# Kernel optimization log

Measured on AMD Instinct MI355X. Metric: run time of the kernel, lower is better.

## Reference

```python
import jax, jax.numpy as jnp
import numpy as np
from jax import lax

DIM = 256
RATE = 4
MAX_SK_IT = 10
N = RATE
NC = N * DIM            # 1024
NG = N * N + 2 * N      # 24


def setup_inputs() -> dict:
    key = jax.random.key(0)
    ks = jax.random.split(key, 5)
    h = jax.random.normal(ks[0], (8, 4096, N, DIM), jnp.float32)
    norm_weight = jax.random.normal(ks[1], (NC,), jnp.float32)
    w = jax.random.normal(ks[2], (NC, NG), jnp.float32) * 0.02
    alpha = jax.random.normal(ks[3], (3,), jnp.float32) * 0.01
    beta = jax.random.normal(ks[4], (NG,), jnp.float32) * 0.1
    return {"h": h, "norm_weight": norm_weight, "w": w, "alpha": alpha, "beta": beta}


def _sinkhorn(K, iters):
    # Sinkhorn-Knopp diagonal scalings u, v such that diag(u) @ K @ diag(v)
    # is (approximately) doubly stochastic. K: (BL, N, N) positive.
    BL, n, _ = K.shape
    u = jnp.ones((BL, n), K.dtype)
    v = jnp.ones((BL, n), K.dtype)

    def body(carry, _):
        u, v = carry
        u = 1.0 / (jnp.einsum('bij,bj->bi', K, v) + 1e-8)
        v = 1.0 / (jnp.einsum('bij,bi->bj', K, u) + 1e-8)
        return (u, v), None

    (u, v), _ = lax.scan(body, (u, v), None, length=iters)
    return u, v


def reference(h, norm_weight, w, alpha, beta):
    B, L, n, D = h.shape
    hf = h.reshape(B, L, n * D)              # (B,L,NC)
    hv = norm_weight * hf                    # mapping uses raw norm weight
    H = hv @ w                               # (B,L,NG)
    r = jnp.linalg.norm(hf, axis=-1, keepdims=True) / np.float32(np.sqrt(n * D))
    r_ = 1.0 / (r + 1e-6)

    H_pre = jax.nn.sigmoid(r_ * H[..., :n] * alpha[0] + beta[:n])            # (B,L,N)
    H_post = 2.0 * jax.nn.sigmoid(r_ * H[..., n:2 * n] * alpha[1] + beta[n:2 * n])
    H_res = (r_ * H[..., 2 * n:] * alpha[2] + beta[2 * n:]).reshape(B, L, n, n)

    K = jnp.exp(H_res).reshape(B * L, n, n)
    u, v = _sinkhorn(K, MAX_SK_IT)
    u = lax.stop_gradient(u)
    v = lax.stop_gradient(v)
    P = (u[:, :, None] * K * v[:, None, :]).reshape(B, L, n, n)

    # process
    h_pre = jnp.einsum('bln,blnd->bld', H_pre, h)[:, :, None, :]  # (B,L,1,D)
    h_res = jnp.einsum('blnm,blmd->blnd', P, h)                   # (B,L,N,D)

    # depth_connection with h_out = h_pre (identity inner layer)
    out = H_post[..., None] * h_pre + h_res                       # (B,L,N,D)
    return out
```

## Files before the change

kernel.cpp:

```cpp
#include <hip/hip_runtime.h>
#include <math.h>


#define NTOK 8

typedef __attribute__((ext_vector_type(2))) _Float16 h2v;

__device__ __forceinline__ float fdot2f(unsigned int a, unsigned int b, float c) {
#if __has_builtin(__builtin_amdgcn_fdot2)
    return __builtin_amdgcn_fdot2(__builtin_bit_cast(h2v, a),
                                  __builtin_bit_cast(h2v, b), c, false);
#else
    h2v av = __builtin_bit_cast(h2v, a);
    h2v bv = __builtin_bit_cast(h2v, b);
    return fmaf((float)av[1], (float)bv[1],
           fmaf((float)av[0], (float)bv[0], c));
#endif
}

__device__ __forceinline__ unsigned int pk_f16(float a, float b) {
    const auto p = __builtin_amdgcn_cvt_pkrtz(a, b);
    return __builtin_bit_cast(unsigned int, p);
}

__device__ __forceinline__ float sigmoid_f(float z) {
    return 1.0f / (1.0f + __expf(-z));
}

__device__ __forceinline__ float row16_sum(float x) {
    x += __int_as_float(__builtin_amdgcn_update_dpp(
        0, __float_as_int(x), 0x121, 0xf, 0xf, false));
    x += __int_as_float(__builtin_amdgcn_update_dpp(
        0, __float_as_int(x), 0x122, 0xf, 0xf, false));
    x += __int_as_float(__builtin_amdgcn_update_dpp(
        0, __float_as_int(x), 0x124, 0xf, 0xf, false));
    x += __int_as_float(__builtin_amdgcn_update_dpp(
        0, __float_as_int(x), 0x128, 0xf, 0xf, false));
    return x;
}

__global__ __launch_bounds__(256)
void prep_kernel(const float* __restrict__ nw,
                 const float* __restrict__ w,
                 const float* __restrict__ alpha,
                 unsigned short* __restrict__ wt)
{
    const int tid = blockIdx.x * 256 + threadIdx.x;
    const int flat = 4 * tid;
    const float4 w4 = *(const float4*)(w + flat);
    const float a0 = alpha[0], a1 = alpha[1], a2 = alpha[2];
    const float vals[4] = {w4.x, w4.y, w4.z, w4.w};
    #pragma unroll
    for (int c = 0; c < 4; ++c) {
        const int f = flat + c;
        const int k = f / 24;
        const int n = f - 24 * k;
        const float as = (n < 4) ? a0 : ((n < 8) ? a1 : a2);
        const unsigned int p = pk_f16(as * nw[k] * vals[c], 0.f);
        wt[n * 1024 + k] = (unsigned short)(p & 0xffffu);
    }
}

__global__ __launch_bounds__(256)
void mhc_kernel(const float* __restrict__ h,
                const unsigned short* __restrict__ wt,
                const float* __restrict__ beta,
                float* __restrict__ out)
{
    const int tid  = threadIdx.x;
    const int lane = tid & 63;
    const int wv   = tid >> 6;
    const int ksl  = lane & 15;
    const int ng   = lane >> 4;

    __shared__ unsigned int tile[NTOK * 512];
    __shared__ float Hpart[NTOK][28];
    __shared__ float smalls[NTOK][26];

    const long tok0 = (long)blockIdx.x * NTOK;

    {
        const float* src = h + tok0 * 1024 + 4 * tid;
        #pragma unroll
        for (int i = 0; i < NTOK; ++i) {
            const float4 v = *(const float4*)(src + 1024 * i);
            uint2 u;
            u.x = pk_f16(v.x, v.y);
            u.y = pk_f16(v.z, v.w);
            *(uint2*)(tile + i * 512 + 2 * tid) = u;
        }
    }
    __syncthreads();

    const int t0 = 2 * wv;
    const uint4* txp = (const uint4*)tile + t0 * 128 + ksl;
    const uint4* twp = (const uint4*)wt + (6 * ng) * 128 + ksl;

    float acc[2][6], r2[2];
    #pragma unroll
    for (int t = 0; t < 2; ++t) {
        r2[t] = 0.f;
        #pragma unroll
        for (int j = 0; j < 6; ++j) acc[t][j] = 0.f;
    }

    #pragma unroll 1
    for (int e = 0; e < 8; ++e) {
        uint4 xw[2];
        #pragma unroll
        for (int t = 0; t < 2; ++t) xw[t] = txp[t * 128 + e * 16];
        uint4 wr[6];
        #pragma unroll
        for (int j = 0; j < 6; ++j) wr[j] = twp[j * 128 + e * 16];

        #pragma unroll
        for (int j = 0; j < 6; ++j) {
            #pragma unroll
            for (int t = 0; t < 2; ++t) {
                float a = acc[t][j];
                a = fdot2f(xw[t].x, wr[j].x, a);
                a = fdot2f(xw[t].y, wr[j].y, a);
                a = fdot2f(xw[t].z, wr[j].z, a);
                a = fdot2f(xw[t].w, wr[j].w, a);
                acc[t][j] = a;
            }
        }
        #pragma unroll
        for (int t = 0; t < 2; ++t) {
            float r = r2[t];
            r = fdot2f(xw[t].x, xw[t].x, r);
            r = fdot2f(xw[t].y, xw[t].y, r);
            r = fdot2f(xw[t].z, xw[t].z, r);
            r = fdot2f(xw[t].w, xw[t].w, r);
            r2[t] = r;
        }
    }

    #pragma unroll
    for (int t = 0; t < 2; ++t) {
        #pragma unroll
        for (int j = 0; j < 6; ++j) acc[t][j] = row16_sum(acc[t][j]);
        r2[t] = row16_sum(r2[t]);
    }
    if (ksl == 0) {
        #pragma unroll
        for (int t = 0; t < 2; ++t) {
            #pragma unroll
            for (int j = 0; j < 6; ++j)
                Hpart[t0 + t][6 * ng + j] = acc[t][j];
            if (ng == 0) Hpart[t0 + t][24] = r2[t];
        }
    }
    __syncthreads();

    if (tid < NTOK) {
        const int t = tid;
        float Hp[24];
        #pragma unroll
        for (int q = 0; q < 24; ++q) Hp[q] = Hpart[t][q];
        const float r2v = Hpart[t][24];
        const float r_ = 1.0f / (sqrtf(r2v) * 0.03125f + 1e-6f);

        float Hpre[4], Hpost[4], K[16];
        #pragma unroll
        for (int n = 0; n < 4; ++n)
            Hpre[n] = sigmoid_f(fmaf(r_, Hp[n], beta[n]));
        #pragma unroll
        for (int n = 0; n < 4; ++n)
            Hpost[n] = 2.0f * sigmoid_f(fmaf(r_, Hp[4 + n], beta[4 + n]));
        #pragma unroll
        for (int q = 0; q < 16; ++q)
            K[q] = __expf(fmaf(r_, Hp[8 + q], beta[8 + q]));

        float u0=1.f,u1=1.f,u2=1.f,u3=1.f;
        float v0=1.f,v1=1.f,v2=1.f,v3=1.f;
        for (int itr = 0; itr < 10; ++itr) {
            u0 = 1.0f/(K[0]*v0  + K[1]*v1  + K[2]*v2  + K[3]*v3  + 1e-8f);
            u1 = 1.0f/(K[4]*v0  + K[5]*v1  + K[6]*v2  + K[7]*v3  + 1e-8f);
            u2 = 1.0f/(K[8]*v0  + K[9]*v1  + K[10]*v2 + K[11]*v3 + 1e-8f);
            u3 = 1.0f/(K[12]*v0 + K[13]*v1 + K[14]*v2 + K[15]*v3 + 1e-8f);
            v0 = 1.0f/(K[0]*u0  + K[4]*u1  + K[8]*u2  + K[12]*u3 + 1e-8f);
            v1 = 1.0f/(K[1]*u0  + K[5]*u1  + K[9]*u2  + K[13]*u3 + 1e-8f);
            v2 = 1.0f/(K[2]*u0  + K[6]*u1  + K[10]*u2 + K[14]*u3 + 1e-8f);
            v3 = 1.0f/(K[3]*u0  + K[7]*u1  + K[11]*u2 + K[15]*u3 + 1e-8f);
        }
        smalls[t][0] = Hpre[0];  smalls[t][1] = Hpre[1];
        smalls[t][2] = Hpre[2];  smalls[t][3] = Hpre[3];
        smalls[t][4] = Hpost[0]; smalls[t][5] = Hpost[1];
        smalls[t][6] = Hpost[2]; smalls[t][7] = Hpost[3];
        smalls[t][8]  = u0*K[0]*v0;   smalls[t][9]  = u0*K[1]*v1;
        smalls[t][10] = u0*K[2]*v2;   smalls[t][11] = u0*K[3]*v3;
        smalls[t][12] = u1*K[4]*v0;   smalls[t][13] = u1*K[5]*v1;
        smalls[t][14] = u1*K[6]*v2;   smalls[t][15] = u1*K[7]*v3;
        smalls[t][16] = u2*K[8]*v0;   smalls[t][17] = u2*K[9]*v1;
        smalls[t][18] = u2*K[10]*v2;  smalls[t][19] = u2*K[11]*v3;
        smalls[t][20] = u3*K[12]*v0;  smalls[t][21] = u3*K[13]*v1;
        smalls[t][22] = u3*K[14]*v2;  smalls[t][23] = u3*K[15]*v3;
    }
    __syncthreads();

    const int gg = wv;
    for (int it = 0; it < NTOK; ++it) {
        const uint2* tl = (const uint2*)tile + it * 256 + lane;
        float xm[4][4];
        #pragma unroll
        for (int m = 0; m < 4; ++m) {
            const uint2 u = tl[m * 64];
            const h2v p0 = __builtin_bit_cast(h2v, u.x);
            const h2v p1 = __builtin_bit_cast(h2v, u.y);
            xm[m][0] = (float)p0[0]; xm[m][1] = (float)p0[1];
            xm[m][2] = (float)p1[0]; xm[m][3] = (float)p1[1];
        }

        const float hp0 = smalls[it][0], hp1 = smalls[it][1];
        const float hp2 = smalls[it][2], hp3 = smalls[it][3];
        const float hpost = smalls[it][4 + gg];
        const float P0 = smalls[it][8 + 4*gg + 0];
        const float P1 = smalls[it][8 + 4*gg + 1];
        const float P2 = smalls[it][8 + 4*gg + 2];
        const float P3 = smalls[it][8 + 4*gg + 3];

        float4 o;
        #pragma unroll
        for (int c = 0; c < 4; ++c) {
            const float hpre = hp0*xm[0][c] + hp1*xm[1][c]
                             + hp2*xm[2][c] + hp3*xm[3][c];
            const float res  = P0*xm[0][c] + P1*xm[1][c]
                             + P2*xm[2][c] + P3*xm[3][c];
            ((float*)&o)[c] = fmaf(hpost, hpre, res);
        }
        *(float4*)(out + (tok0 + it) * 1024 + gg * 256 + 4 * lane) = o;
    }
}

extern "C" void kernel_launch(void* const* d_in, const int* in_sizes, int n_in,
                              void* d_out, int out_size, void* d_ws, size_t ws_size,
                              hipStream_t stream) {
    const float* h     = (const float*)d_in[0];
    const float* nw    = (const float*)d_in[1];
    const float* w     = (const float*)d_in[2];
    const float* alpha = (const float*)d_in[3];
    const float* beta  = (const float*)d_in[4];
    float* out = (float*)d_out;
    unsigned short* wt = (unsigned short*)d_ws;

    prep_kernel<<<24, 256, 0, stream>>>(nw, w, alpha, wt);
    mhc_kernel<<<4096, 256, 0, stream>>>(h, wt, beta, out);
}
```

Baseline: 68.31 us.

## Double-buffer token tiles so each block prefetches the next 8 tokens during GEMV

Each block now handles 16 tokens in two halves of 8, with two LDS tiles. While the first half's projection dot products run, the global loads for the second half are issued in two batches and converted into the other tile. The grid is halved and launch bounds request 3 blocks per CU. The aim is to hide global load latency behind compute. The cost is more LDS per block, more registers and fewer blocks in flight, so there is less latency hiding from occupancy.

```diff
diff --git a/kernel.cpp b/kernel.cpp
--- a/kernel.cpp
+++ b/kernel.cpp
@@ -1,8 +1,6 @@
 #include <hip/hip_runtime.h>
 #include <math.h>
 
-
-#define NTOK 8
 
 typedef __attribute__((ext_vector_type(2))) _Float16 h2v;
 
@@ -61,7 +59,7 @@
     }
 }
 
-__global__ __launch_bounds__(256)
+__global__ __launch_bounds__(256, 3)
 void mhc_kernel(const float* __restrict__ h,
                 const unsigned short* __restrict__ wt,
                 const float* __restrict__ beta,
@@ -73,163 +71,240 @@
     const int ksl  = lane & 15;
     const int ng   = lane >> 4;
 
-    __shared__ unsigned int tile[NTOK * 512];
-    __shared__ float Hpart[NTOK][28];
-    __shared__ float smalls[NTOK][26];
-
-    const long tok0 = (long)blockIdx.x * NTOK;
+    __shared__ unsigned int tileA[8 * 512];
+    __shared__ unsigned int tileB[8 * 512];
+    __shared__ float Hpart[8][28];
+    __shared__ float smalls[8][26];
+
+    const long tokbase = (long)blockIdx.x * 16;
 
     {
-        const float* src = h + tok0 * 1024 + 4 * tid;
-        #pragma unroll
-        for (int i = 0; i < NTOK; ++i) {
+        const float* src = h + tokbase * 1024 + 4 * tid;
+        #pragma unroll
+        for (int i = 0; i < 8; ++i) {
             const float4 v = *(const float4*)(src + 1024 * i);
             uint2 u;
             u.x = pk_f16(v.x, v.y);
             u.y = pk_f16(v.z, v.w);
-            *(uint2*)(tile + i * 512 + 2 * tid) = u;
+            *(uint2*)(tileA + i * 512 + 2 * tid) = u;
         }
     }
     __syncthreads();
 
-    const int t0 = 2 * wv;
-    const uint4* txp = (const uint4*)tile + t0 * 128 + ksl;
-    const uint4* twp = (const uint4*)wt + (6 * ng) * 128 + ksl;
-
-    float acc[2][6], r2[2];
     #pragma unroll
     for (int t = 0; t < 2; ++t) {
-        r2[t] = 0.f;
-        #pragma unroll
-        for (int j = 0; j < 6; ++j) acc[t][j] = 0.f;
-    }
-
-    #pragma unroll 1
-    for (int e = 0; e < 8; ++e) {
-        uint4 xw[2];
-        #pragma unroll
-        for (int t = 0; t < 2; ++t) xw[t] = txp[t * 128 + e * 16];
-        uint4 wr[6];
-        #pragma unroll
-        for (int j = 0; j < 6; ++j) wr[j] = twp[j * 128 + e * 16];
-
-        #pragma unroll
-        for (int j = 0; j < 6; ++j) {
-            #pragma unroll
-            for (int t = 0; t < 2; ++t) {
-                float a = acc[t][j];
-                a = fdot2f(xw[t].x, wr[j].x, a);
-                a = fdot2f(xw[t].y, wr[j].y, a);
-                a = fdot2f(xw[t].z, wr[j].z, a);
-                a = fdot2f(xw[t].w, wr[j].w, a);
-                acc[t][j] = a;
-            }
-        }
-        #pragma unroll
-        for (int t = 0; t < 2; ++t) {
-            float r = r2[t];
-            r = fdot2f(xw[t].x, xw[t].x, r);
-            r = fdot2f(xw[t].y, xw[t].y, r);
-            r = fdot2f(xw[t].z, xw[t].z, r);
-            r = fdot2f(xw[t].w, xw[t].w, r);
-            r2[t] = r;
-        }
-    }
-
-    #pragma unroll
-    for (int t = 0; t < 2; ++t) {
-        #pragma unroll
-        for (int j = 0; j < 6; ++j) acc[t][j] = row16_sum(acc[t][j]);
-        r2[t] = row16_sum(r2[t]);
-    }
-    if (ksl == 0) {
-        #pragma unroll
-        for (int t = 0; t < 2; ++t) {
-            #pragma unroll
-            for (int j = 0; j < 6; ++j)
-                Hpart[t0 + t][6 * ng + j] = acc[t][j];
-            if (ng == 0) Hpart[t0 + t][24] = r2[t];
-        }
-    }
-    __syncthreads();
-
-    if (tid < NTOK) {
-        const int t = tid;
-        float Hp[24];
-        #pragma unroll
-        for (int q = 0; q < 24; ++q) Hp[q] = Hpart[t][q];
-        const float r2v = Hpart[t][24];
-        const float r_ = 1.0f / (sqrtf(r2v) * 0.03125f + 1e-6f);
-
-        float Hpre[4], Hpost[4], K[16];
-        #pragma unroll
-        for (int n = 0; n < 4; ++n)
-            Hpre[n] = sigmoid_f(fmaf(r_, Hp[n], beta[n]));
-        #pragma unroll
-        for (int n = 0; n < 4; ++n)
-            Hpost[n] = 2.0f * sigmoid_f(fmaf(r_, Hp[4 + n], beta[4 + n]));
-        #pragma unroll
-        for (int q = 0; q < 16; ++q)
-            K[q] = __expf(fmaf(r_, Hp[8 + q], beta[8 + q]));
-
-        float u0=1.f,u1=1.f,u2=1.f,u3=1.f;
-        float v0=1.f,v1=1.f,v2=1.f,v3=1.f;
-        for (int itr = 0; itr < 10; ++itr) {
-            u0 = 1.0f/(K[0]*v0  + K[1]*v1  + K[2]*v2  + K[3]*v3  + 1e-8f);
-            u1 = 1.0f/(K[4]*v0  + K[5]*v1  + K[6]*v2  + K[7]*v3  + 1e-8f);
-            u2 = 1.0f/(K[8]*v0  + K[9]*v1  + K[10]*v2 + K[11]*v3 + 1e-8f);
-            u3 = 1.0f/(K[12]*v0 + K[13]*v1 + K[14]*v2 + K[15]*v3 + 1e-8f);
-            v0 = 1.0f/(K[0]*u0  + K[4]*u1  + K[8]*u2  + K[12]*u3 + 1e-8f);
-            v1 = 1.0f/(K[1]*u0  + K[5]*u1  + K[9]*u2  + K[13]*u3 + 1e-8f);
-            v2 = 1.0f/(K[2]*u0  + K[6]*u1  + K[10]*u2 + K[14]*u3 + 1e-8f);
-            v3 = 1.0f/(K[3]*u0  + K[7]*u1  + K[11]*u2 + K[15]*u3 + 1e-8f);
-        }
-        smalls[t][0] = Hpre[0];  smalls[t][1] = Hpre[1];
-        smalls[t][2] = Hpre[2];  smalls[t][3] = Hpre[3];
-        smalls[t][4] = Hpost[0]; smalls[t][5] = Hpost[1];
-        smalls[t][6] = Hpost[2]; smalls[t][7] = Hpost[3];
-        smalls[t][8]  = u0*K[0]*v0;   smalls[t][9]  = u0*K[1]*v1;
-        smalls[t][10] = u0*K[2]*v2;   smalls[t][11] = u0*K[3]*v3;
-        smalls[t][12] = u1*K[4]*v0;   smalls[t][13] = u1*K[5]*v1;
-        smalls[t][14] = u1*K[6]*v2;   smalls[t][15] = u1*K[7]*v3;
-        smalls[t][16] = u2*K[8]*v0;   smalls[t][17] = u2*K[9]*v1;
-        smalls[t][18] = u2*K[10]*v2;  smalls[t][19] = u2*K[11]*v3;
-        smalls[t][20] = u3*K[12]*v0;  smalls[t][21] = u3*K[13]*v1;
-        smalls[t][22] = u3*K[14]*v2;  smalls[t][23] = u3*K[15]*v3;
-    }
-    __syncthreads();
-
-    const int gg = wv;
-    for (int it = 0; it < NTOK; ++it) {
-        const uint2* tl = (const uint2*)tile + it * 256 + lane;
-        float xm[4][4];
-        #pragma unroll
-        for (int m = 0; m < 4; ++m) {
-            const uint2 u = tl[m * 64];
-            const h2v p0 = __builtin_bit_cast(h2v, u.x);
-            const h2v p1 = __builtin_bit_cast(h2v, u.y);
-            xm[m][0] = (float)p0[0]; xm[m][1] = (float)p0[1];
-            xm[m][2] = (float)p1[0]; xm[m][3] = (float)p1[1];
-        }
-
-        const float hp0 = smalls[it][0], hp1 = smalls[it][1];
-        const float hp2 = smalls[it][2], hp3 = smalls[it][3];
-        const float hpost = smalls[it][4 + gg];
-        const float P0 = smalls[it][8 + 4*gg + 0];
-        const float P1 = smalls[it][8 + 4*gg + 1];
-        const float P2 = smalls[it][8 + 4*gg + 2];
-        const float P3 = smalls[it][8 + 4*gg + 3];
-
-        float4 o;
-        #pragma unroll
-        for (int c = 0; c < 4; ++c) {
-            const float hpre = hp0*xm[0][c] + hp1*xm[1][c]
-                             + hp2*xm[2][c] + hp3*xm[3][c];
-            const float res  = P0*xm[0][c] + P1*xm[1][c]
-                             + P2*xm[2][c] + P3*xm[3][c];
-            ((float*)&o)[c] = fmaf(hpost, hpre, res);
-        }
-        *(float4*)(out + (tok0 + it) * 1024 + gg * 256 + 4 * lane) = o;
+        unsigned int* cur = (t == 0) ? tileA : tileB;
+        unsigned int* nxt = (t == 0) ? tileB : tileA;
+        const bool has_next = (t == 0);
+        const long tok0 = tokbase + t * 8;
+        const float* src2 = h + (tok0 + 8) * 1024 + 4 * tid;
+
+        const int t0 = 2 * wv;
+        const uint4* txp = (const uint4*)cur + t0 * 128 + ksl;
+        const uint4* twp = (const uint4*)wt + (6 * ng) * 128 + ksl;
+
+        float acc[2][6], r2[2];
+        #pragma unroll
+        for (int tt = 0; tt < 2; ++tt) {
+            r2[tt] = 0.f;
+            #pragma unroll
+            for (int j = 0; j < 6; ++j) acc[tt][j] = 0.f;
+        }
+
+        float4 st0, st1, st2, st3;
+        if (has_next) {
+            st0 = *(const float4*)(src2);
+            st1 = *(const float4*)(src2 + 1024);
+            st2 = *(const float4*)(src2 + 2048);
+            st3 = *(const float4*)(src2 + 3072);
+        }
+
+        #pragma unroll
+        for (int e = 0; e < 4; ++e) {
+            uint4 xw[2];
+            #pragma unroll
+            for (int tt = 0; tt < 2; ++tt) xw[tt] = txp[tt * 128 + e * 16];
+            uint4 wr[6];
+            #pragma unroll
+            for (int j = 0; j < 6; ++j) wr[j] = twp[j * 128 + e * 16];
+            #pragma unroll
+            for (int j = 0; j < 6; ++j) {
+                #pragma unroll
+                for (int tt = 0; tt < 2; ++tt) {
+                    float a = acc[tt][j];
+                    a = fdot2f(xw[tt].x, wr[j].x, a);
+                    a = fdot2f(xw[tt].y, wr[j].y, a);
+                    a = fdot2f(xw[tt].z, wr[j].z, a);
+                    a = fdot2f(xw[tt].w, wr[j].w, a);
+                    acc[tt][j] = a;
+                }
+            }
+            #pragma unroll
+            for (int tt = 0; tt < 2; ++tt) {
+                float r = r2[tt];
+                r = fdot2f(xw[tt].x, xw[tt].x, r);
+                r = fdot2f(xw[tt].y, xw[tt].y, r);
+                r = fdot2f(xw[tt].z, xw[tt].z, r);
+                r = fdot2f(xw[tt].w, xw[tt].w, r);
+                r2[tt] = r;
+            }
+        }
+
+        if (has_next) {
+            uint2 u;
+            u.x = pk_f16(st0.x, st0.y); u.y = pk_f16(st0.z, st0.w);
+            *(uint2*)(nxt + 0 * 512 + 2 * tid) = u;
+            u.x = pk_f16(st1.x, st1.y); u.y = pk_f16(st1.z, st1.w);
+            *(uint2*)(nxt + 1 * 512 + 2 * tid) = u;
+            u.x = pk_f16(st2.x, st2.y); u.y = pk_f16(st2.z, st2.w);
+            *(uint2*)(nxt + 2 * 512 + 2 * tid) = u;
+            u.x = pk_f16(st3.x, st3.y); u.y = pk_f16(st3.z, st3.w);
+            *(uint2*)(nxt + 3 * 512 + 2 * tid) = u;
+            st0 = *(const float4*)(src2 + 4096);
+            st1 = *(const float4*)(src2 + 5120);
+            st2 = *(const float4*)(src2 + 6144);
+            st3 = *(const float4*)(src2 + 7168);
+        }
+
+        #pragma unroll
+        for (int e = 4; e < 8; ++e) {
+            uint4 xw[2];
+            #pragma unroll
+            for (int tt = 0; tt < 2; ++tt) xw[tt] = txp[tt * 128 + e * 16];
+            uint4 wr[6];
+            #pragma unroll
+            for (int j = 0; j < 6; ++j) wr[j] = twp[j * 128 + e * 16];
+            #pragma unroll
+            for (int j = 0; j < 6; ++j) {
+                #pragma unroll
+                for (int tt = 0; tt < 2; ++tt) {
+                    float a = acc[tt][j];
+                    a = fdot2f(xw[tt].x, wr[j].x, a);
+                    a = fdot2f(xw[tt].y, wr[j].y, a);
+                    a = fdot2f(xw[tt].z, wr[j].z, a);
+                    a = fdot2f(xw[tt].w, wr[j].w, a);
+                    acc[tt][j] = a;
+                }
+            }
+            #pragma unroll
+            for (int tt = 0; tt < 2; ++tt) {
+                float r = r2[tt];
+                r = fdot2f(xw[tt].x, xw[tt].x, r);
+                r = fdot2f(xw[tt].y, xw[tt].y, r);
+                r = fdot2f(xw[tt].z, xw[tt].z, r);
+                r = fdot2f(xw[tt].w, xw[tt].w, r);
+                r2[tt] = r;
+            }
+        }
+
+        if (has_next) {
+            uint2 u;
+            u.x = pk_f16(st0.x, st0.y); u.y = pk_f16(st0.z, st0.w);
+            *(uint2*)(nxt + 4 * 512 + 2 * tid) = u;
+            u.x = pk_f16(st1.x, st1.y); u.y = pk_f16(st1.z, st1.w);
+            *(uint2*)(nxt + 5 * 512 + 2 * tid) = u;
+            u.x = pk_f16(st2.x, st2.y); u.y = pk_f16(st2.z, st2.w);
+            *(uint2*)(nxt + 6 * 512 + 2 * tid) = u;
+            u.x = pk_f16(st3.x, st3.y); u.y = pk_f16(st3.z, st3.w);
+            *(uint2*)(nxt + 7 * 512 + 2 * tid) = u;
+        }
+
+        #pragma unroll
+        for (int tt = 0; tt < 2; ++tt) {
+            #pragma unroll
+            for (int j = 0; j < 6; ++j) acc[tt][j] = row16_sum(acc[tt][j]);
+            r2[tt] = row16_sum(r2[tt]);
+        }
+        if (ksl == 0) {
+            #pragma unroll
+            for (int tt = 0; tt < 2; ++tt) {
+                #pragma unroll
+                for (int j = 0; j < 6; ++j)
+                    Hpart[t0 + tt][6 * ng + j] = acc[tt][j];
+                if (ng == 0) Hpart[t0 + tt][24] = r2[tt];
+            }
+        }
+        __syncthreads();
+
+        if (tid < 8) {
+            const int tk = tid;
+            float Hp[24];
+            #pragma unroll
+            for (int q = 0; q < 24; ++q) Hp[q] = Hpart[tk][q];
+            const float r2v = Hpart[tk][24];
+            const float r_ = 1.0f / (sqrtf(r2v) * 0.03125f + 1e-6f);
+
+            float Hpre[4], Hpost[4], K[16];
+            #pragma unroll
+            for (int n = 0; n < 4; ++n)
+                Hpre[n] = sigmoid_f(fmaf(r_, Hp[n], beta[n]));
+            #pragma unroll
+            for (int n = 0; n < 4; ++n)
+                Hpost[n] = 2.0f * sigmoid_f(fmaf(r_, Hp[4 + n], beta[4 + n]));
+            #pragma unroll
+            for (int q = 0; q < 16; ++q)
+                K[q] = __expf(fmaf(r_, Hp[8 + q], beta[8 + q]));
+
+            float u0=1.f,u1=1.f,u2=1.f,u3=1.f;
+            float v0=1.f,v1=1.f,v2=1.f,v3=1.f;
+            for (int itr = 0; itr < 10; ++itr) {
+                u0 = 1.0f/(K[0]*v0  + K[1]*v1  + K[2]*v2  + K[3]*v3  + 1e-8f);
+                u1 = 1.0f/(K[4]*v0  + K[5]*v1  + K[6]*v2  + K[7]*v3  + 1e-8f);
+                u2 = 1.0f/(K[8]*v0  + K[9]*v1  + K[10]*v2 + K[11]*v3 + 1e-8f);
+                u3 = 1.0f/(K[12]*v0 + K[13]*v1 + K[14]*v2 + K[15]*v3 + 1e-8f);
+                v0 = 1.0f/(K[0]*u0  + K[4]*u1  + K[8]*u2  + K[12]*u3 + 1e-8f);
+                v1 = 1.0f/(K[1]*u0  + K[5]*u1  + K[9]*u2  + K[13]*u3 + 1e-8f);
+                v2 = 1.0f/(K[2]*u0  + K[6]*u1  + K[10]*u2 + K[14]*u3 + 1e-8f);
+                v3 = 1.0f/(K[3]*u0  + K[7]*u1  + K[11]*u2 + K[15]*u3 + 1e-8f);
+            }
+            smalls[tk][0] = Hpre[0];  smalls[tk][1] = Hpre[1];
+            smalls[tk][2] = Hpre[2];  smalls[tk][3] = Hpre[3];
+            smalls[tk][4] = Hpost[0]; smalls[tk][5] = Hpost[1];
+            smalls[tk][6] = Hpost[2]; smalls[tk][7] = Hpost[3];
+            smalls[tk][8]  = u0*K[0]*v0;   smalls[tk][9]  = u0*K[1]*v1;
+            smalls[tk][10] = u0*K[2]*v2;   smalls[tk][11] = u0*K[3]*v3;
+            smalls[tk][12] = u1*K[4]*v0;   smalls[tk][13] = u1*K[5]*v1;
+            smalls[tk][14] = u1*K[6]*v2;   smalls[tk][15] = u1*K[7]*v3;
+            smalls[tk][16] = u2*K[8]*v0;   smalls[tk][17] = u2*K[9]*v1;
+            smalls[tk][18] = u2*K[10]*v2;  smalls[tk][19] = u2*K[11]*v3;
+            smalls[tk][20] = u3*K[12]*v0;  smalls[tk][21] = u3*K[13]*v1;
+            smalls[tk][22] = u3*K[14]*v2;  smalls[tk][23] = u3*K[15]*v3;
+        }
+        __syncthreads();
+
+        const int gg = wv;
+        for (int it = 0; it < 8; ++it) {
+            const uint2* tl = (const uint2*)cur + it * 256 + lane;
+            float xm[4][4];
+            #pragma unroll
+            for (int m = 0; m < 4; ++m) {
+                const uint2 u = tl[m * 64];
+                const h2v p0 = __builtin_bit_cast(h2v, u.x);
+                const h2v p1 = __builtin_bit_cast(h2v, u.y);
+                xm[m][0] = (float)p0[0]; xm[m][1] = (float)p0[1];
+                xm[m][2] = (float)p1[0]; xm[m][3] = (float)p1[1];
+            }
+
+            const float hp0 = smalls[it][0], hp1 = smalls[it][1];
+            const float hp2 = smalls[it][2], hp3 = smalls[it][3];
+            const float hpost = smalls[it][4 + gg];
+            const float P0 = smalls[it][8 + 4*gg + 0];
+            const float P1 = smalls[it][8 + 4*gg + 1];
+            const float P2 = smalls[it][8 + 4*gg + 2];
+            const float P3 = smalls[it][8 + 4*gg + 3];
+
+            float4 o;
+            #pragma unroll
+            for (int c = 0; c < 4; ++c) {
+                const float hpre = hp0*xm[0][c] + hp1*xm[1][c]
+                                 + hp2*xm[2][c] + hp3*xm[3][c];
+                const float res  = P0*xm[0][c] + P1*xm[1][c]
+                                 + P2*xm[2][c] + P3*xm[3][c];
+                ((float*)&o)[c] = fmaf(hpost, hpre, res);
+            }
+            *(float4*)(out + (tok0 + it) * 1024 + gg * 256 + 4 * lane) = o;
+        }
+        __syncthreads();
     }
 }
 
@@ -245,5 +320,5 @@
     unsigned short* wt = (unsigned short*)d_ws;
 
     prep_kernel<<<24, 256, 0, stream>>>(nw, w, alpha, wt);
-    mhc_kernel<<<4096, 256, 0, stream>>>(h, wt, beta, out);
-}
+    mhc_kernel<<<2048, 256, 0, stream>>>(h, wt, beta, out);
+}
```

Result: slower. 83.82 us (+22.7%).
